# Performance work log

Hardware: AMD Instinct MI355X
Metric: run time of the kernel (lower is better)

## Reference

```python
import jax, jax.numpy as jnp
import numpy as np


def _lstm_cell(x, h, c, W_ih, W_hh, b_ih, b_hh):
    # torch gate order: input, forget, cell(g), output
    g = x @ W_ih.T + h @ W_hh.T + b_ih + b_hh
    i, f, gg, o = jnp.split(g, 4, axis=-1)
    c_new = jax.nn.sigmoid(f) * c + jax.nn.sigmoid(i) * jnp.tanh(gg)
    h_new = jax.nn.sigmoid(o) * jnp.tanh(c_new)
    return h_new, c_new


def setup_inputs() -> dict:
    key = jax.random.key(0)
    ks = jax.random.split(key, 11)
    T, B, D, E, H, V = 64, 4096, 32, 32, 5, 10
    IN = D + 3 * E  # 128 = input_size
    s = 0.1
    return {
        "horizon": T,
        "hidden": jax.random.normal(ks[0], (2, B, H), jnp.float32),
        "cell": jax.random.normal(ks[1], (2, B, H), jnp.float32),
        "dec_x": jax.random.normal(ks[2], (T, B, D), jnp.float32),
        "mote_id_cat": jax.random.randint(ks[3], (T, B), 0, V),
        "fault_type_cat": jax.random.randint(ks[4], (T, B), 0, V),
        "mote_fault_cat": jax.random.randint(ks[5], (T, B), 0, V),
        "mote_embed": jax.random.normal(ks[6], (V, E), jnp.float32),
        "W_ih0": jax.random.normal(ks[7], (4 * H, IN), jnp.float32) * s,
        "W_hh0": jax.random.normal(ks[8], (4 * H, H), jnp.float32) * s,
        "b_ih0": jnp.zeros((4 * H,), jnp.float32),
        "b_hh0": jnp.zeros((4 * H,), jnp.float32),
        "W_ih1": jax.random.normal(ks[9], (4 * H, H), jnp.float32) * s,
        "W_hh1": jax.random.normal(ks[10], (4 * H, H), jnp.float32) * s,
        "b_ih1": jnp.zeros((4 * H,), jnp.float32),
        "b_hh1": jnp.zeros((4 * H,), jnp.float32),
    }


def reference(horizon, hidden, cell, dec_x, mote_id_cat, fault_type_cat,
              mote_fault_cat, mote_embed, W_ih0, W_hh0, b_ih0, b_hh0,
              W_ih1, W_hh1, b_ih1, b_hh1):
    # Faithful to source: ALL three categorical features use mote_embed.
    e1 = mote_embed[mote_id_cat]      # [T,B,E]
    e2 = mote_embed[fault_type_cat]   # [T,B,E]
    e3 = mote_embed[mote_fault_cat]   # [T,B,E]
    x = jnp.concatenate([dec_x, e1, e2, e3], axis=-1)[:horizon]  # [T,B,IN]

    # Source re-feeds the SAME initial (hidden, cell) at every horizon step,
    # so steps are independent -> vmap over time (no carried recurrence).
    def step(xt):  # xt: [B, IN]
        h1, _ = _lstm_cell(xt, hidden[0], cell[0], W_ih0, W_hh0, b_ih0, b_hh0)
        h2, _ = _lstm_cell(h1, hidden[1], cell[1], W_ih1, W_hh1, b_ih1, b_hh1)
        return h2  # top-layer output, [B, H]

    return jax.vmap(step)(x)  # [T, B, H]
```

## Files before the change

### kernel.cpp

```cpp
#include <hip/hip_runtime.h>
#include <math.h>

#define HDIM 5
#define GATES 20
#define DDIM 32
#define EDIM 32
#define INDIM 128
#define VOC 10
#define SPN (3 * VOC * GATES)
#define HH_OFF 1024

__device__ __forceinline__ float sigmoidf_(float x) {
    return __builtin_amdgcn_rcpf(1.0f + __expf(-x));
}
__device__ __forceinline__ float tanhf_(float x) {
    float e = __expf(-2.0f * x);
    return fmaf(2.0f, __builtin_amdgcn_rcpf(1.0f + e), -1.0f);
}

__global__ __launch_bounds__(256) void precompute_kernel(
    const float* __restrict__ hidden,
    const float* __restrict__ emb,
    const float* __restrict__ W_ih0,
    const float* __restrict__ W_hh0, const float* __restrict__ b_ih0,
    const float* __restrict__ b_hh0,
    const float* __restrict__ W_hh1, const float* __restrict__ b_ih1,
    const float* __restrict__ b_hh1,
    float* __restrict__ ws, int B)
{
    int gid = blockIdx.x * 256 + threadIdx.x;
    if (gid < SPN) {
        int s = gid / (VOC * GATES);
        int rem = gid % (VOC * GATES);
        int v = rem / GATES, r = rem % GATES;
        const float4* ev = (const float4*)(emb + v * EDIM);
        const float4* wv = (const float4*)(W_ih0 + r * INDIM + DDIM + s * EDIM);
        float a = 0.0f;
        #pragma unroll
        for (int k = 0; k < EDIM / 4; ++k) {
            float4 e4 = ev[k], w4 = wv[k];
            a = fmaf(e4.x, w4.x, a); a = fmaf(e4.y, w4.y, a);
            a = fmaf(e4.z, w4.z, a); a = fmaf(e4.w, w4.w, a);
        }
        ws[gid] = a;
    }
    if (gid < B) {
        float h0[HDIM], h1v[HDIM];
        #pragma unroll
        for (int h = 0; h < HDIM; ++h) {
            h0[h]  = hidden[(size_t)gid * HDIM + h];
            h1v[h] = hidden[((size_t)B + gid) * HDIM + h];
        }
        #pragma unroll
        for (int r = 0; r < GATES; ++r) {
            float a0 = b_ih0[r] + b_hh0[r];
            float a1 = b_ih1[r] + b_hh1[r];
            #pragma unroll
            for (int h = 0; h < HDIM; ++h) {
                a0 = fmaf(h0[h],  W_hh0[r * HDIM + h], a0);
                a1 = fmaf(h1v[h], W_hh1[r * HDIM + h], a1);
            }
            ws[HH_OFF + (size_t)gid * GATES + r] = a0;
            ws[HH_OFF + (size_t)(B + gid) * GATES + r] = a1;
        }
    }
}

__global__ __launch_bounds__(256, 4) void decoder_kernel(
    const float* __restrict__ cell,
    const float* __restrict__ dec_x,
    const int*   __restrict__ midc,
    const int*   __restrict__ ftc,
    const int*   __restrict__ mfc,
    const float* __restrict__ W_ih0,
    const float* __restrict__ W_ih1,
    const float* __restrict__ ws,
    float* __restrict__ out,
    int B, int total)
{
    __shared__ float sP[SPN];
    for (int j = threadIdx.x; j < SPN; j += 256) sP[j] = ws[j];
    __syncthreads();

    const int idx = blockIdx.x * 256 + threadIdx.x;
    if (idx >= total) return;
    const int t = idx / B;
    const int b = idx - t * B;
    (void)t;

    const float4* xp = (const float4*)dec_x + (size_t)idx * (DDIM / 4);
    float4 x[DDIM / 4];
    #pragma unroll
    for (int k = 0; k < DDIM / 4; ++k) x[k] = xp[k];

    const int vm = midc[idx], vf = ftc[idx], vmf = mfc[idx];

    float acc[GATES];
    const float4* hh0p = (const float4*)(ws + HH_OFF + (size_t)b * GATES);
    #pragma unroll
    for (int k = 0; k < 5; ++k) {
        float4 h4 = hh0p[k];
        acc[4 * k + 0] = h4.x; acc[4 * k + 1] = h4.y;
        acc[4 * k + 2] = h4.z; acc[4 * k + 3] = h4.w;
    }

    const float4* P0 = (const float4*)(sP + vm * GATES);
    const float4* P1 = (const float4*)(sP + VOC * GATES + vf * GATES);
    const float4* P2 = (const float4*)(sP + 2 * VOC * GATES + vmf * GATES);
    #pragma unroll
    for (int k = 0; k < 5; ++k) {
        float4 p0 = P0[k], p1 = P1[k], p2 = P2[k];
        acc[4 * k + 0] += p0.x + p1.x + p2.x;
        acc[4 * k + 1] += p0.y + p1.y + p2.y;
        acc[4 * k + 2] += p0.z + p1.z + p2.z;
        acc[4 * k + 3] += p0.w + p1.w + p2.w;
    }

    #pragma unroll
    for (int r = 0; r < GATES; ++r) {
        const float* w = W_ih0 + r * INDIM;
        float a = acc[r];
        #pragma unroll
        for (int k = 0; k < DDIM / 4; ++k) {
            a = fmaf(x[k].x, w[4 * k + 0], a);
            a = fmaf(x[k].y, w[4 * k + 1], a);
            a = fmaf(x[k].z, w[4 * k + 2], a);
            a = fmaf(x[k].w, w[4 * k + 3], a);
        }
        acc[r] = a;
    }

    float h1[HDIM];
    #pragma unroll
    for (int r = 0; r < HDIM; ++r) {
        float c0 = cell[(size_t)b * HDIM + r];
        float ii = sigmoidf_(acc[r]);
        float ff = sigmoidf_(acc[HDIM + r]);
        float gg = tanhf_(acc[2 * HDIM + r]);
        float oo = sigmoidf_(acc[3 * HDIM + r]);
        float cn = fmaf(ff, c0, ii * gg);
        h1[r] = oo * tanhf_(cn);
    }

    float g1[GATES];
    const float4* hh1p = (const float4*)(ws + HH_OFF + (size_t)(B + b) * GATES);
    #pragma unroll
    for (int k = 0; k < 5; ++k) {
        float4 h4 = hh1p[k];
        g1[4 * k + 0] = h4.x; g1[4 * k + 1] = h4.y;
        g1[4 * k + 2] = h4.z; g1[4 * k + 3] = h4.w;
    }
    #pragma unroll
    for (int r = 0; r < GATES; ++r) {
        float a = g1[r];
        #pragma unroll
        for (int h = 0; h < HDIM; ++h)
            a = fmaf(h1[h], W_ih1[r * HDIM + h], a);
        g1[r] = a;
    }

    #pragma unroll
    for (int r = 0; r < HDIM; ++r) {
        float c1 = cell[((size_t)B + b) * HDIM + r];
        float ii = sigmoidf_(g1[r]);
        float ff = sigmoidf_(g1[HDIM + r]);
        float gg = tanhf_(g1[2 * HDIM + r]);
        float oo = sigmoidf_(g1[3 * HDIM + r]);
        float cn = fmaf(ff, c1, ii * gg);
        out[(size_t)idx * HDIM + r] = oo * tanhf_(cn);
    }
}

extern "C" void kernel_launch(void* const* d_in, const int* in_sizes, int n_in,
                              void* d_out, int out_size, void* d_ws, size_t ws_size,
                              hipStream_t stream) {
    const float* hidden = (const float*)d_in[1];
    const float* cellp  = (const float*)d_in[2];
    const float* dec_x  = (const float*)d_in[3];
    const int*   midc   = (const int*)d_in[4];
    const int*   ftc    = (const int*)d_in[5];
    const int*   mfc    = (const int*)d_in[6];
    const float* emb    = (const float*)d_in[7];
    const float* W_ih0  = (const float*)d_in[8];
    const float* W_hh0  = (const float*)d_in[9];
    const float* b_ih0  = (const float*)d_in[10];
    const float* b_hh0  = (const float*)d_in[11];
    const float* W_ih1  = (const float*)d_in[12];
    const float* W_hh1  = (const float*)d_in[13];
    const float* b_ih1  = (const float*)d_in[14];
    const float* b_hh1  = (const float*)d_in[15];
    float* out = (float*)d_out;
    float* ws  = (float*)d_ws;

    int B = in_sizes[1] / (2 * HDIM);
    int horizon = out_size / (B * HDIM);
    int total = horizon * B;

    int pre_n = (B > SPN ? B : SPN);
    int pre_grid = (pre_n + 255) / 256;
    precompute_kernel<<<pre_grid, 256, 0, stream>>>(
        hidden, emb, W_ih0, W_hh0, b_ih0, b_hh0, W_hh1, b_ih1, b_hh1, ws, B);

    int grid = (total + 255) / 256;
    if (grid < 1) grid = 1;
    decoder_kernel<<<grid, 256, 0, stream>>>(
        cellp, dec_x, midc, ftc, mfc, W_ih0, W_ih1, ws, out, B, total);
}
```

Measured before the change: 118.8 us.

## Fuse precompute into decoder kernel, recompute hidden projections per thread

Removes the separate precompute kernel. Each block now builds the embedding-projection table directly in shared memory, and each thread recomputes the W_hh·h plus bias terms from the hidden state instead of reading precomputed gate vectors from workspace. This saves one kernel launch, the dependency between the two kernels, and the workspace write and read traffic. In exchange, every block redoes the 600-entry table computation and every thread does extra FMAs with broadcast weight loads.

```diff
diff --git a/kernel.cpp b/kernel.cpp
--- a/kernel.cpp
+++ b/kernel.cpp
@@ -8,7 +8,6 @@
 #define INDIM 128
 #define VOC 10
 #define SPN (3 * VOC * GATES)
-#define HH_OFF 1024
 
 __device__ __forceinline__ float sigmoidf_(float x) {
     return __builtin_amdgcn_rcpf(1.0f + __expf(-x));
@@ -18,21 +17,30 @@
     return fmaf(2.0f, __builtin_amdgcn_rcpf(1.0f + e), -1.0f);
 }
 
-__global__ __launch_bounds__(256) void precompute_kernel(
+__global__ __launch_bounds__(256, 4) void decoder_fused(
     const float* __restrict__ hidden,
+    const float* __restrict__ cell,
+    const float* __restrict__ dec_x,
+    const int*   __restrict__ midc,
+    const int*   __restrict__ ftc,
+    const int*   __restrict__ mfc,
     const float* __restrict__ emb,
     const float* __restrict__ W_ih0,
-    const float* __restrict__ W_hh0, const float* __restrict__ b_ih0,
+    const float* __restrict__ W_hh0,
+    const float* __restrict__ b_ih0,
     const float* __restrict__ b_hh0,
-    const float* __restrict__ W_hh1, const float* __restrict__ b_ih1,
+    const float* __restrict__ W_ih1,
+    const float* __restrict__ W_hh1,
+    const float* __restrict__ b_ih1,
     const float* __restrict__ b_hh1,
-    float* __restrict__ ws, int B)
+    float* __restrict__ out,
+    int B, int total)
 {
-    int gid = blockIdx.x * 256 + threadIdx.x;
-    if (gid < SPN) {
-        int s = gid / (VOC * GATES);
-        int rem = gid % (VOC * GATES);
-        int v = rem / GATES, r = rem % GATES;
+    __shared__ float sP[SPN];
+    for (int j = threadIdx.x; j < SPN; j += 256) {
+        int s = j / (VOC * GATES);
+        int rem = j - s * (VOC * GATES);
+        int v = rem / GATES, r = rem - v * GATES;
         const float4* ev = (const float4*)(emb + v * EDIM);
         const float4* wv = (const float4*)(W_ih0 + r * INDIM + DDIM + s * EDIM);
         float a = 0.0f;
@@ -42,66 +50,31 @@
             a = fmaf(e4.x, w4.x, a); a = fmaf(e4.y, w4.y, a);
             a = fmaf(e4.z, w4.z, a); a = fmaf(e4.w, w4.w, a);
         }
-        ws[gid] = a;
+        sP[j] = a;
     }
-    if (gid < B) {
-        float h0[HDIM], h1v[HDIM];
-        #pragma unroll
-        for (int h = 0; h < HDIM; ++h) {
-            h0[h]  = hidden[(size_t)gid * HDIM + h];
-            h1v[h] = hidden[((size_t)B + gid) * HDIM + h];
-        }
-        #pragma unroll
-        for (int r = 0; r < GATES; ++r) {
-            float a0 = b_ih0[r] + b_hh0[r];
-            float a1 = b_ih1[r] + b_hh1[r];
-            #pragma unroll
-            for (int h = 0; h < HDIM; ++h) {
-                a0 = fmaf(h0[h],  W_hh0[r * HDIM + h], a0);
-                a1 = fmaf(h1v[h], W_hh1[r * HDIM + h], a1);
-            }
-            ws[HH_OFF + (size_t)gid * GATES + r] = a0;
-            ws[HH_OFF + (size_t)(B + gid) * GATES + r] = a1;
-        }
-    }
-}
-
-__global__ __launch_bounds__(256, 4) void decoder_kernel(
-    const float* __restrict__ cell,
-    const float* __restrict__ dec_x,
-    const int*   __restrict__ midc,
-    const int*   __restrict__ ftc,
-    const int*   __restrict__ mfc,
-    const float* __restrict__ W_ih0,
-    const float* __restrict__ W_ih1,
-    const float* __restrict__ ws,
-    float* __restrict__ out,
-    int B, int total)
-{
-    __shared__ float sP[SPN];
-    for (int j = threadIdx.x; j < SPN; j += 256) sP[j] = ws[j];
     __syncthreads();
 
     const int idx = blockIdx.x * 256 + threadIdx.x;
     if (idx >= total) return;
-    const int t = idx / B;
-    const int b = idx - t * B;
-    (void)t;
+    const int b = (int)((unsigned)idx % (unsigned)B);
 
     const float4* xp = (const float4*)dec_x + (size_t)idx * (DDIM / 4);
     float4 x[DDIM / 4];
     #pragma unroll
     for (int k = 0; k < DDIM / 4; ++k) x[k] = xp[k];
-
     const int vm = midc[idx], vf = ftc[idx], vmf = mfc[idx];
 
+    float h0[HDIM];
+    #pragma unroll
+    for (int h = 0; h < HDIM; ++h) h0[h] = hidden[(size_t)b * HDIM + h];
+
     float acc[GATES];
-    const float4* hh0p = (const float4*)(ws + HH_OFF + (size_t)b * GATES);
     #pragma unroll
-    for (int k = 0; k < 5; ++k) {
-        float4 h4 = hh0p[k];
-        acc[4 * k + 0] = h4.x; acc[4 * k + 1] = h4.y;
-        acc[4 * k + 2] = h4.z; acc[4 * k + 3] = h4.w;
+    for (int r = 0; r < GATES; ++r) {
+        float a = b_ih0[r] + b_hh0[r];
+        #pragma unroll
+        for (int h = 0; h < HDIM; ++h) a = fmaf(h0[h], W_hh0[r * HDIM + h], a);
+        acc[r] = a;
     }
 
     const float4* P0 = (const float4*)(sP + vm * GATES);
@@ -142,17 +115,16 @@
         h1[r] = oo * tanhf_(cn);
     }
 
+    float h1v[HDIM];
+    #pragma unroll
+    for (int h = 0; h < HDIM; ++h) h1v[h] = hidden[((size_t)B + b) * HDIM + h];
     float g1[GATES];
-    const float4* hh1p = (const float4*)(ws + HH_OFF + (size_t)(B + b) * GATES);
-    #pragma unroll
-    for (int k = 0; k < 5; ++k) {
-        float4 h4 = hh1p[k];
-        g1[4 * k + 0] = h4.x; g1[4 * k + 1] = h4.y;
-        g1[4 * k + 2] = h4.z; g1[4 * k + 3] = h4.w;
-    }
     #pragma unroll
     for (int r = 0; r < GATES; ++r) {
-        float a = g1[r];
+        float a = b_ih1[r] + b_hh1[r];
+        #pragma unroll
+        for (int h = 0; h < HDIM; ++h)
+            a = fmaf(h1v[h], W_hh1[r * HDIM + h], a);
         #pragma unroll
         for (int h = 0; h < HDIM; ++h)
             a = fmaf(h1[h], W_ih1[r * HDIM + h], a);
@@ -190,19 +162,16 @@
     const float* b_ih1  = (const float*)d_in[14];
     const float* b_hh1  = (const float*)d_in[15];
     float* out = (float*)d_out;
-    float* ws  = (float*)d_ws;
+    (void)d_ws; (void)ws_size;
 
     int B = in_sizes[1] / (2 * HDIM);
     int horizon = out_size / (B * HDIM);
     int total = horizon * B;
 
-    int pre_n = (B > SPN ? B : SPN);
-    int pre_grid = (pre_n + 255) / 256;
-    precompute_kernel<<<pre_grid, 256, 0, stream>>>(
-        hidden, emb, W_ih0, W_hh0, b_ih0, b_hh0, W_hh1, b_ih1, b_hh1, ws, B);
-
     int grid = (total + 255) / 256;
     if (grid < 1) grid = 1;
-    decoder_kernel<<<grid, 256, 0, stream>>>(
-        cellp, dec_x, midc, ftc, mfc, W_ih0, W_ih1, ws, out, B, total);
+    decoder_fused<<<grid, 256, 0, stream>>>(
+        hidden, cellp, dec_x, midc, ftc, mfc, emb,
+        W_ih0, W_hh0, b_ih0, b_hh0, W_ih1, W_hh1, b_ih1, b_hh1,
+        out, B, total);
 }
```

Result: slower. 122.6 us (+3.2%).
